# Optimization experiments

Hardware: AMD Instinct MI355X
Metric: run time of the kernel (lower is better)

## Reference

```python
import jax, jax.numpy as jnp
import numpy as np

N = 50000      # nodes
E = 800000     # edges (avg degree 16)
IN = 256       # in_feats
H = 128        # hidden_feats
C = 40         # out_feats == num classes (label dim)
LPA_ITERS = 10


def setup_inputs() -> dict:
    key = jax.random.key(0)
    ks = jax.random.split(key, 9)
    features = jax.random.normal(ks[0], (N, IN), dtype=jnp.float32)
    labels = jax.random.normal(ks[1], (N, C), dtype=jnp.float32)
    mask = jax.random.randint(ks[2], (N,), 0, 2) > 0          # bool [N]
    src = jax.random.randint(ks[3], (E,), 0, N, dtype=jnp.int32)
    dst = jax.random.randint(ks[4], (E,), 0, N, dtype=jnp.int32)
    W1 = jax.random.normal(ks[5], (IN, H), dtype=jnp.float32) * (1.0 / np.sqrt(IN))
    b1 = jnp.zeros((H,), dtype=jnp.float32)
    W2 = jax.random.normal(ks[6], (H, C), dtype=jnp.float32) * (1.0 / np.sqrt(H))
    b2 = jnp.zeros((C,), dtype=jnp.float32)
    return {"features": features, "labels": labels, "mask": mask,
            "src": src, "dst": dst, "W1": W1, "b1": b1, "W2": W2, "b2": b2}


def reference(features, labels, mask, src, dst, W1, b1, W2, b2):
    ones_e = jnp.ones((E,), dtype=jnp.float32)
    deg_out = jax.ops.segment_sum(ones_e, src, num_segments=N)  # out-degree
    deg_in = jax.ops.segment_sum(ones_e, dst, num_segments=N)   # in-degree
    norm_src = jnp.maximum(deg_out, 1.0) ** -0.5                 # DGL clamps deg>=1
    norm_dst = jnp.maximum(deg_in, 1.0) ** -0.5

    def gconv(x, W, b):
        # DGL GraphConv, norm='both': D_in^{-1/2} A^T D_out^{-1/2} (x W) + b
        h = (x @ W) * norm_src[:, None]                          # [N, d_out]
        agg = jax.ops.segment_sum(h[src], dst, num_segments=N)   # gather+scatter-add
        return agg * norm_dst[:, None] + b

    x = jax.nn.relu(gconv(features, W1, b1))
    # dropout identity in eval mode
    x = gconv(x, W2, b2)

    # Label propagation: adj[src,dst]=1 so (adj @ y)[i] = sum_{(i->j)} y[j]
    masked_labels = jnp.where(mask[:, None], labels, 0.0)

    def step(y, _):
        y = jax.ops.segment_sum(y[dst], src, num_segments=N)
        y = jnp.where(mask[:, None], labels, y)
        return y, None

    y, _ = jax.lax.scan(step, masked_labels, None, length=LPA_ITERS)
    return x, y
```

## Files before the change

### kernel.cpp

```cpp
#include <hip/hip_runtime.h>

#define Nn 50000
#define Ee 800000
#define INF_ 256
#define HID 128
#define NC 40
#define CAPD 48
#define CAPS 48
#define LPA_ITERS 10
#define NB 98
#define BSH 9
#define EPB 1024
#define NBLK ((Ee + EPB - 1) / EPB)
#define CAPB_D 10240
#define CAPB_S 6144

typedef __attribute__((ext_vector_type(8))) short bfrag;
typedef __attribute__((ext_vector_type(4))) float ffrag;

__device__ inline unsigned f2bf2(float a, float b) {
    unsigned ua = __float_as_uint(a); ua += 0x7FFFu + ((ua >> 16) & 1u);
    unsigned ub = __float_as_uint(b); ub += 0x7FFFu + ((ub >> 16) & 1u);
    return (ua >> 16) | (ub & 0xFFFF0000u);
}
__device__ inline unsigned short f2bf(float a) {
    unsigned ua = __float_as_uint(a); ua += 0x7FFFu + ((ua >> 16) & 1u);
    return (unsigned short)(ua >> 16);
}
__device__ inline float bf_lo(unsigned u) { return __uint_as_float(u << 16); }
__device__ inline float bf_hi(unsigned u) { return __uint_as_float(u & 0xFFFF0000u); }

__global__ void detect_fmt(const unsigned int* __restrict__ m, int* flag) {
    int i = blockIdx.x * blockDim.x + threadIdx.x;
    if (i < 12500) {
        if (m[i] > 1u) atomicOr(flag, 1);
    }
}

__device__ inline bool read_mask(const void* mask, int node, int fmt) {
    if (fmt) return ((const unsigned char*)mask)[node] != 0;
    return ((const int*)mask)[node] != 0;
}

__global__ __launch_bounds__(256) void bin_edges(
    const int* __restrict__ src, const int* __restrict__ dst,
    const void* __restrict__ mask, const int* __restrict__ flag,
    int* __restrict__ cnt_src,
    int* __restrict__ cur_d, int* __restrict__ cur_s,
    unsigned* __restrict__ bkt_d, unsigned* __restrict__ bkt_s) {
    __shared__ unsigned stage_d[EPB];
    __shared__ unsigned stage_s[EPB];
    __shared__ int hd[NB], od[NB + 1], cd[NB], gd_[NB];
    __shared__ int hs[NB], os_[NB + 1], cs_[NB], gs_[NB];
    __shared__ int sc[256];
    int tid = threadIdx.x;
    int e0 = blockIdx.x * EPB;
    int fmt = *flag;
    if (tid < NB) { hd[tid] = 0; hs[tid] = 0; }
    __syncthreads();

    int rs[EPB / 256], rd[EPB / 256];
    unsigned um = 0;
#pragma unroll
    for (int k = 0; k < EPB / 256; k++) {
        int e = e0 + tid + k * 256;
        rs[k] = -1; rd[k] = -1;
        if (e < Ee) {
            int s = src[e], d = dst[e];
            rs[k] = s; rd[k] = d;
            atomicAdd(&cnt_src[s], 1);
            atomicAdd(&hd[d >> BSH], 1);
            if (!read_mask(mask, s, fmt)) {
                um |= (1u << k);
                atomicAdd(&hs[s >> BSH], 1);
            }
        }
    }
    __syncthreads();
    {
        int seg = tid >> 7;
        int i = tid & 127;
        int v = 0;
        if (i < NB) v = seg ? hs[i] : hd[i];
        sc[tid] = v;
        __syncthreads();
#pragma unroll
        for (int offs = 1; offs < 128; offs <<= 1) {
            int add = (i >= offs) ? sc[tid - offs] : 0;
            __syncthreads();
            sc[tid] += add;
            __syncthreads();
        }
        if (i < NB) {
            int excl = i ? sc[tid - 1] : 0;
            if (seg == 0) od[i] = excl; else os_[i] = excl;
            if (i == NB - 1) {
                if (seg == 0) od[NB] = sc[tid]; else os_[NB] = sc[tid];
            }
        }
    }
    __syncthreads();
    if (tid < NB) {
        gd_[tid] = hd[tid] ? atomicAdd(&cur_d[tid], hd[tid]) : 0;
        gs_[tid] = hs[tid] ? atomicAdd(&cur_s[tid], hs[tid]) : 0;
        cd[tid] = od[tid];
        cs_[tid] = os_[tid];
    }
    __syncthreads();
#pragma unroll
    for (int k = 0; k < EPB / 256; k++) {
        if (rd[k] >= 0) {
            int p = atomicAdd(&cd[rd[k] >> BSH], 1);
            stage_d[p] = ((unsigned)rd[k] << 16) | (unsigned)rs[k];
            if (um & (1u << k)) {
                int q = atomicAdd(&cs_[rs[k] >> BSH], 1);
                stage_s[q] = ((unsigned)rs[k] << 16) | (unsigned)rd[k];
            }
        }
    }
    __syncthreads();
    int totd = od[NB];
    for (int i = tid; i < totd; i += 256) {
        int lo = 0, hi = NB;
        while (hi - lo > 1) {
            int mid = (lo + hi) >> 1;
            if (od[mid] <= i) lo = mid; else hi = mid;
        }
        int pos = gd_[lo] + (i - od[lo]);
        if (pos < CAPB_D) bkt_d[(size_t)lo * CAPB_D + pos] = stage_d[i];
    }
    int tots = os_[NB];
    for (int i = tid; i < tots; i += 256) {
        int lo = 0, hi = NB;
        while (hi - lo > 1) {
            int mid = (lo + hi) >> 1;
            if (os_[mid] <= i) lo = mid; else hi = mid;
        }
        int pos = gs_[lo] + (i - os_[lo]);
        if (pos < CAPB_S) bkt_s[(size_t)lo * CAPB_S + pos] = stage_s[i];
    }
}

__global__ __launch_bounds__(256) void build_csr_both(
    const unsigned* __restrict__ bkt_d, const int* __restrict__ cur_d,
    const unsigned* __restrict__ bkt_s, const int* __restrict__ cur_s,
    const void* __restrict__ mask, const int* __restrict__ flag,
    int* __restrict__ adj_dst, int* __restrict__ cnt_dst,
    int* __restrict__ adj_s, int* __restrict__ cnt_u, int* __restrict__ cnt_m) {
    __shared__ int lu[512], lm[512];
    int bb = blockIdx.x, tid = threadIdx.x;
    lu[tid] = 0; lu[tid + 256] = 0; lm[tid] = 0; lm[tid + 256] = 0;
    __syncthreads();
    if (bb < NB) {
        int b = bb;
        int n = cur_d[b]; if (n > CAPB_D) n = CAPB_D;
        int n0 = b << BSH;
        const unsigned* base = bkt_d + (size_t)b * CAPB_D;
        for (int i = tid; i < n; i += 256) {
            unsigned r = base[i];
            int d = r >> 16, s = r & 0xffff;
            int sl = atomicAdd(&lu[d - n0], 1);
            if (sl < CAPD) adj_dst[d * CAPD + sl] = s;
        }
        __syncthreads();
        int g0 = n0 + tid;
        if (g0 < Nn) cnt_dst[g0] = lu[tid];
        g0 += 256;
        if (g0 < Nn) cnt_dst[g0] = lu[tid + 256];
    } else {
        int b = bb - NB;
        int fmt = *flag;
        int n = cur_s[b]; if (n > CAPB_S) n = CAPB_S;
        int n0 = b << BSH;
        const unsigned* base = bkt_s + (size_t)b * CAPB_S;
        for (int i = tid; i < n; i += 256) {
            unsigned r = base[i];
            int s = r >> 16, d = r & 0xffff;
            if (read_mask(mask, d, fmt)) {
                int sl = atomicAdd(&lm[s - n0], 1);
                if (sl < CAPS) adj_s[s * CAPS + (CAPS - 1 - sl)] = d;
            } else {
                int sl = atomicAdd(&lu[s - n0], 1);
                if (sl < CAPS) adj_s[s * CAPS + sl] = d;
            }
        }
        __syncthreads();
        int g0 = n0 + tid;
        if (g0 < Nn) { cnt_u[g0] = lu[tid]; cnt_m[g0] = lm[tid]; }
        g0 += 256;
        if (g0 < Nn) { cnt_u[g0] = lu[tid + 256]; cnt_m[g0] = lm[tid + 256]; }
    }
}

__global__ void build_unmasked(const void* __restrict__ mask,
                               const int* __restrict__ flag,
                               int* n_un, int* __restrict__ ulist) {
    int i = blockIdx.x * blockDim.x + threadIdx.x;
    if (i < Nn) {
        if (!read_mask(mask, i, *flag)) {
            int p = atomicAdd(n_un, 1);
            ulist[p] = i;
        }
    }
}

__global__ void prep_w1t(const float* __restrict__ W1,
                         unsigned short* __restrict__ W1t) {
    int c = blockIdx.x;
    int k = threadIdx.x;
    W1t[c * INF_ + k] = f2bf(W1[(size_t)k * HID + c]);
}

#define G1_ROWS 64
__global__ __launch_bounds__(256) void gemm1(
    const float* __restrict__ feat, const unsigned short* __restrict__ W1t,
    const int* __restrict__ cnt_src, unsigned short* __restrict__ h1b) {
    __shared__ unsigned short lA[G1_ROWS * 32];
    __shared__ unsigned short lB[HID * 32];
    const int tid = threadIdx.x;
    const int row0 = blockIdx.x * G1_ROWS;
    const int w = tid >> 6;
    const int l = tid & 63;
    const int lane15 = l & 15;
    const int quad = l >> 4;
    const int rw0 = w * 16;

    ffrag acc[8];
#pragma unroll
    for (int t = 0; t < 8; t++) acc[t] = (ffrag){0.f, 0.f, 0.f, 0.f};

    for (int k0 = 0; k0 < INF_; k0 += 32) {
#pragma unroll
        for (int p = 0; p < 2; p++) {
            int idx = tid + p * 256;
            int r = idx >> 3, c4 = idx & 7;
            int grow = row0 + r;
            float4 v = make_float4(0.f, 0.f, 0.f, 0.f);
            if (grow < Nn)
                v = *(const float4*)(feat + (size_t)grow * INF_ + k0 + c4 * 4);
            uint2 pk;
            pk.x = f2bf2(v.x, v.y);
            pk.y = f2bf2(v.z, v.w);
            *(uint2*)((char*)lA + r * 64 + c4 * 8) = pk;
        }
#pragma unroll
        for (int p = 0; p < 2; p++) {
            int idx = tid + p * 256;
            int col = idx >> 2, q = idx & 3;
            uint4 v = *(const uint4*)((const char*)W1t + col * 512 + k0 * 2 + q * 16);
            *(uint4*)((char*)lB + col * 64 + q * 16) = v;
        }
        __syncthreads();
        int arow = rw0 + lane15;
        bfrag af = *(const bfrag*)((const char*)lA + arow * 64 + quad * 16);
#pragma unroll
        for (int t = 0; t < 8; t++) {
            int col = t * 16 + lane15;
            bfrag bf = *(const bfrag*)((const char*)lB + col * 64 + quad * 16);
            acc[t] = __builtin_amdgcn_mfma_f32_16x16x32_bf16(af, bf, acc[t], 0, 0, 0);
        }
        __syncthreads();
    }
    float nrm[4];
#pragma unroll
    for (int i = 0; i < 4; i++) {
        int grow = row0 + rw0 + quad * 4 + i;
        int dg = (grow < Nn) ? cnt_src[grow] : 1;
        nrm[i] = rsqrtf((float)(dg > 1 ? dg : 1));
    }
#pragma unroll
    for (int t = 0; t < 8; t++) {
#pragma unroll
        for (int i = 0; i < 4; i++) {
            int grow = row0 + rw0 + quad * 4 + i;
            if (grow < Nn)
                h1b[(size_t)grow * HID + t * 16 + lane15] = f2bf(acc[t][i] * nrm[i]);
        }
    }
}

__global__ __launch_bounds__(256) void agg_relu1(
    const uint4* __restrict__ h1b, const int* __restrict__ adj_dst,
    const int* __restrict__ cnt_dst, const float4* __restrict__ b1,
    float4* __restrict__ x1) {
    int node = blockIdx.x * 16 + (threadIdx.x >> 4);
    int l = threadIdx.x & 15;
    int dg = cnt_dst[node];
    int cnt = dg < CAPD ? dg : CAPD;
    const int* lst = adj_dst + (size_t)node * CAPD;
    float s0 = 0.f, s1 = 0.f, s2 = 0.f, s3 = 0.f;
    float s4 = 0.f, s5 = 0.f, s6 = 0.f, s7 = 0.f;
    int e = 0;
    for (; e + 8 <= cnt; e += 8) {
        uint4 u[8];
#pragma unroll
        for (int q = 0; q < 8; q++) u[q] = h1b[(size_t)lst[e + q] * 16 + l];
#pragma unroll
        for (int q = 0; q < 8; q++) {
            s0 += bf_lo(u[q].x); s1 += bf_hi(u[q].x);
            s2 += bf_lo(u[q].y); s3 += bf_hi(u[q].y);
            s4 += bf_lo(u[q].z); s5 += bf_hi(u[q].z);
            s6 += bf_lo(u[q].w); s7 += bf_hi(u[q].w);
        }
    }
    for (; e < cnt; e++) {
        uint4 u = h1b[(size_t)lst[e] * 16 + l];
        s0 += bf_lo(u.x); s1 += bf_hi(u.x);
        s2 += bf_lo(u.y); s3 += bf_hi(u.y);
        s4 += bf_lo(u.z); s5 += bf_hi(u.z);
        s6 += bf_lo(u.w); s7 += bf_hi(u.w);
    }
    float nrm = rsqrtf((float)(dg > 1 ? dg : 1));
    float4 bb0 = b1[l * 2], bb1 = b1[l * 2 + 1];
    float4 v0, v1;
    v0.x = fmaxf(s0 * nrm + bb0.x, 0.f);
    v0.y = fmaxf(s1 * nrm + bb0.y, 0.f);
    v0.z = fmaxf(s2 * nrm + bb0.z, 0.f);
    v0.w = fmaxf(s3 * nrm + bb0.w, 0.f);
    v1.x = fmaxf(s4 * nrm + bb1.x, 0.f);
    v1.y = fmaxf(s5 * nrm + bb1.y, 0.f);
    v1.z = fmaxf(s6 * nrm + bb1.z, 0.f);
    v1.w = fmaxf(s7 * nrm + bb1.w, 0.f);
    x1[(size_t)node * 32 + l * 2] = v0;
    x1[(size_t)node * 32 + l * 2 + 1] = v1;
}

__global__ __launch_bounds__(256) void gemm2(
    const float4* __restrict__ x1, const float4* __restrict__ W2,
    const int* __restrict__ cnt_src, unsigned* __restrict__ h2b) {
    __shared__ float lw[HID * NC];
    int tid = threadIdx.x;
    for (int i = tid; i < HID * NC / 4; i += 256)
        ((float4*)lw)[i] = W2[i];
    __syncthreads();
    int r = blockIdx.x * 256 + tid;
    if (r >= Nn) return;
    const float4* xr = x1 + (size_t)r * 32;
    float4 acc[10];
#pragma unroll
    for (int j = 0; j < 10; j++) acc[j] = make_float4(0.f, 0.f, 0.f, 0.f);
    for (int k4 = 0; k4 < 32; k4++) {
        float4 xv = xr[k4];
#pragma unroll
        for (int s = 0; s < 4; s++) {
            float x = s == 0 ? xv.x : (s == 1 ? xv.y : (s == 2 ? xv.z : xv.w));
            const float4* wrow = (const float4*)(lw + (k4 * 4 + s) * NC);
#pragma unroll
            for (int j = 0; j < 10; j++) {
                float4 w = wrow[j];
                acc[j].x += x * w.x; acc[j].y += x * w.y;
                acc[j].z += x * w.z; acc[j].w += x * w.w;
            }
        }
    }
    int dg = cnt_src[r];
    float nrm = rsqrtf((float)(dg > 1 ? dg : 1));
    uint2* out = (uint2*)(h2b + (size_t)r * 20);
#pragma unroll
    for (int j = 0; j < 10; j++) {
        uint2 pk;
        pk.x = f2bf2(acc[j].x * nrm, acc[j].y * nrm);
        pk.y = f2bf2(acc[j].z * nrm, acc[j].w * nrm);
        out[j] = pk;
    }
}

__global__ __launch_bounds__(320) void agg2(
    const uint2* __restrict__ h2b, const int* __restrict__ adj_dst,
    const int* __restrict__ cnt_dst, const float4* __restrict__ b2,
    float4* __restrict__ out_x) {
    int node = blockIdx.x * 32 + threadIdx.x / 10;
    int l = threadIdx.x % 10;
    if (node >= Nn) return;
    int dg = cnt_dst[node];
    int cnt = dg < CAPD ? dg : CAPD;
    const int* lst = adj_dst + (size_t)node * CAPD;
    float s0 = 0.f, s1 = 0.f, s2 = 0.f, s3 = 0.f;
    int e = 0;
    for (; e + 8 <= cnt; e += 8) {
        uint2 u[8];
#pragma unroll
        for (int q = 0; q < 8; q++) u[q] = h2b[(size_t)lst[e + q] * 10 + l];
#pragma unroll
        for (int q = 0; q < 8; q++) {
            s0 += bf_lo(u[q].x); s1 += bf_hi(u[q].x);
            s2 += bf_lo(u[q].y); s3 += bf_hi(u[q].y);
        }
    }
    for (; e + 4 <= cnt; e += 4) {
        uint2 u[4];
#pragma unroll
        for (int q = 0; q < 4; q++) u[q] = h2b[(size_t)lst[e + q] * 10 + l];
#pragma unroll
        for (int q = 0; q < 4; q++) {
            s0 += bf_lo(u[q].x); s1 += bf_hi(u[q].x);
            s2 += bf_lo(u[q].y); s3 += bf_hi(u[q].y);
        }
    }
    for (; e < cnt; e++) {
        uint2 u = h2b[(size_t)lst[e] * 10 + l];
        s0 += bf_lo(u.x); s1 += bf_hi(u.x);
        s2 += bf_lo(u.y); s3 += bf_hi(u.y);
    }
    float nrm = rsqrtf((float)(dg > 1 ? dg : 1));
    float4 bb = b2[l];
    float4 v;
    v.x = s0 * nrm + bb.x;
    v.y = s1 * nrm + bb.y;
    v.z = s2 * nrm + bb.z;
    v.w = s3 * nrm + bb.w;
    out_x[(size_t)node * 10 + l] = v;
}

__global__ void lpa_init(const float* __restrict__ labels, const void* mask,
                         const int* __restrict__ flag, float* __restrict__ out_y) {
    int g = blockIdx.x * blockDim.x + threadIdx.x;
    if (g >= Nn * NC) return;
    int node = g / NC;
    if (read_mask(mask, node, *flag)) out_y[g] = labels[g];
}

__global__ __launch_bounds__(320) void lpa_const(
    const float4* __restrict__ labels, const int* __restrict__ n_un,
    const int* __restrict__ ulist, const int* __restrict__ adj_s,
    const int* __restrict__ cnt_m, float4* __restrict__ sconst,
    uint2* __restrict__ y1b) {
    int g = blockIdx.x * 32 + threadIdx.x / 10;
    int l = threadIdx.x % 10;
    if (g >= *n_un) return;
    int u = ulist[g];
    int cm = cnt_m[u];
    int cnt = cm < CAPS ? cm : CAPS;
    const int* lst = adj_s + (size_t)u * CAPS + (CAPS - cnt);
    float4 s = make_float4(0.f, 0.f, 0.f, 0.f);
    int e = 0;
    for (; e + 8 <= cnt; e += 8) {
        float4 v[8];
#pragma unroll
        for (int q = 0; q < 8; q++) v[q] = labels[(size_t)lst[e + q] * 10 + l];
#pragma unroll
        for (int q = 0; q < 8; q++) {
            s.x += v[q].x; s.y += v[q].y; s.z += v[q].z; s.w += v[q].w;
        }
    }
    for (; e + 4 <= cnt; e += 4) {
        float4 v[4];
#pragma unroll
        for (int q = 0; q < 4; q++) v[q] = labels[(size_t)lst[e + q] * 10 + l];
#pragma unroll
        for (int q = 0; q < 4; q++) {
            s.x += v[q].x; s.y += v[q].y; s.z += v[q].z; s.w += v[q].w;
        }
    }
    for (; e < cnt; e++) {
        float4 a = labels[(size_t)lst[e] * 10 + l];
        s.x += a.x; s.y += a.y; s.z += a.z; s.w += a.w;
    }
    sconst[(size_t)u * 10 + l] = s;
    uint2 pk; pk.x = f2bf2(s.x, s.y); pk.y = f2bf2(s.z, s.w);
    y1b[(size_t)u * 10 + l] = pk;
}

__global__ __launch_bounds__(320) void lpa_mid(
    const uint2* __restrict__ ycur, const int* __restrict__ n_un,
    const int* __restrict__ ulist, const int* __restrict__ adj_s,
    const int* __restrict__ cnt_u, const float4* __restrict__ sconst,
    uint2* __restrict__ ynext) {
    int g = blockIdx.x * 32 + threadIdx.x / 10;
    int l = threadIdx.x % 10;
    if (g >= *n_un) return;
    int u = ulist[g];
    int cu = cnt_u[u];
    int cnt = cu < CAPS ? cu : CAPS;
    const int* lst = adj_s + (size_t)u * CAPS;
    float4 s = sconst[(size_t)u * 10 + l];
    int e = 0;
    for (; e + 8 <= cnt; e += 8) {
        uint2 v[8];
#pragma unroll
        for (int q = 0; q < 8; q++) v[q] = ycur[(size_t)lst[e + q] * 10 + l];
#pragma unroll
        for (int q = 0; q < 8; q++) {
            s.x += bf_lo(v[q].x); s.y += bf_hi(v[q].x);
            s.z += bf_lo(v[q].y); s.w += bf_hi(v[q].y);
        }
    }
    for (; e + 4 <= cnt; e += 4) {
        uint2 v[4];
#pragma unroll
        for (int q = 0; q < 4; q++) v[q] = ycur[(size_t)lst[e + q] * 10 + l];
#pragma unroll
        for (int q = 0; q < 4; q++) {
            s.x += bf_lo(v[q].x); s.y += bf_hi(v[q].x);
            s.z += bf_lo(v[q].y); s.w += bf_hi(v[q].y);
        }
    }
    for (; e < cnt; e++) {
        uint2 v = ycur[(size_t)lst[e] * 10 + l];
        s.x += bf_lo(v.x); s.y += bf_hi(v.x);
        s.z += bf_lo(v.y); s.w += bf_hi(v.y);
    }
    uint2 pk; pk.x = f2bf2(s.x, s.y); pk.y = f2bf2(s.z, s.w);
    ynext[(size_t)u * 10 + l] = pk;
}

__global__ __launch_bounds__(320) void lpa_last(
    const uint2* __restrict__ ycur, const int* __restrict__ n_un,
    const int* __restrict__ ulist, const int* __restrict__ adj_s,
    const int* __restrict__ cnt_u, const float4* __restrict__ sconst,
    float4* __restrict__ out_y) {
    int g = blockIdx.x * 32 + threadIdx.x / 10;
    int l = threadIdx.x % 10;
    if (g >= *n_un) return;
    int u = ulist[g];
    int cu = cnt_u[u];
    int cnt = cu < CAPS ? cu : CAPS;
    const int* lst = adj_s + (size_t)u * CAPS;
    float4 s = sconst[(size_t)u * 10 + l];
    int e = 0;
    for (; e + 8 <= cnt; e += 8) {
        uint2 v[8];
#pragma unroll
        for (int q = 0; q < 8; q++) v[q] = ycur[(size_t)lst[e + q] * 10 + l];
#pragma unroll
        for (int q = 0; q < 8; q++) {
            s.x += bf_lo(v[q].x); s.y += bf_hi(v[q].x);
            s.z += bf_lo(v[q].y); s.w += bf_hi(v[q].y);
        }
    }
    for (; e + 4 <= cnt; e += 4) {
        uint2 v[4];
#pragma unroll
        for (int q = 0; q < 4; q++) v[q] = ycur[(size_t)lst[e + q] * 10 + l];
#pragma unroll
        for (int q = 0; q < 4; q++) {
            s.x += bf_lo(v[q].x); s.y += bf_hi(v[q].x);
            s.z += bf_lo(v[q].y); s.w += bf_hi(v[q].y);
        }
    }
    for (; e < cnt; e++) {
        uint2 v = ycur[(size_t)lst[e] * 10 + l];
        s.x += bf_lo(v.x); s.y += bf_hi(v.x);
        s.z += bf_lo(v.y); s.w += bf_hi(v.y);
    }
    out_y[(size_t)u * 10 + l] = s;
}

extern "C" void kernel_launch(void* const* d_in, const int* in_sizes, int n_in,
                              void* d_out, int out_size, void* d_ws, size_t ws_size,
                              hipStream_t stream) {
    const float* feat   = (const float*)d_in[0];
    const float* labels = (const float*)d_in[1];
    const void*  mask   = d_in[2];
    const int*   src    = (const int*)d_in[3];
    const int*   dst    = (const int*)d_in[4];
    const float* W1     = (const float*)d_in[5];
    const float* b1     = (const float*)d_in[6];
    const float* W2     = (const float*)d_in[7];
    const float* b2     = (const float*)d_in[8];

    float* out_x = (float*)d_out;
    float* out_y = out_x + (size_t)Nn * NC;

    char* ws = (char*)d_ws;
    size_t off = 0;
    auto alloc = [&](size_t bytes) -> void* {
        void* p = ws + off;
        off += (bytes + 255) & ~(size_t)255;
        return p;
    };
    int* flag    = (int*)alloc(256);
    int* n_un    = flag + 1;
    int* cnt_src = (int*)alloc((size_t)Nn * 4);
    int* cur_d   = (int*)alloc(512);
    int* cur_s   = (int*)alloc(512);
    size_t zero_bytes = off;
    int* cnt_dst = (int*)alloc((size_t)Nn * 4);
    int* cnt_u   = (int*)alloc((size_t)Nn * 4);
    int* cnt_m   = (int*)alloc((size_t)Nn * 4);
    int* ulist   = (int*)alloc((size_t)Nn * 4);
    unsigned short* W1t = (unsigned short*)alloc((size_t)HID * INF_ * 2);
    char* uni = (char*)alloc((size_t)Nn * HID * 2);
    unsigned* bkt_d = (unsigned*)uni;
    unsigned* bkt_s = (unsigned*)(uni + (size_t)NB * CAPB_D * 4);
    unsigned short* h1b = (unsigned short*)uni;
    float* x1 = (float*)alloc((size_t)Nn * HID * 4);
    int* adj_s   = (int*)alloc((size_t)Nn * CAPS * 4);
    int* adj_dst = (int*)alloc((size_t)Nn * CAPD * 4);
    unsigned* h2b = (unsigned*)alloc((size_t)Nn * NC * 2);
    float* sconst = (float*)alloc((size_t)Nn * NC * 4);
    uint2* y1b = (uint2*)alloc((size_t)Nn * NC * 2);
    uint2* y2b = (uint2*)alloc((size_t)Nn * NC * 2);

    hipMemsetAsync(d_ws, 0, zero_bytes, stream);

    detect_fmt<<<49, 256, 0, stream>>>((const unsigned int*)mask, flag);
    prep_w1t<<<HID, INF_, 0, stream>>>(W1, W1t);
    bin_edges<<<NBLK, 256, 0, stream>>>(src, dst, mask, flag, cnt_src,
                                        cur_d, cur_s, bkt_d, bkt_s);
    build_csr_both<<<NB * 2, 256, 0, stream>>>(bkt_d, cur_d, bkt_s, cur_s,
                                               mask, flag, adj_dst, cnt_dst,
                                               adj_s, cnt_u, cnt_m);
    build_unmasked<<<196, 256, 0, stream>>>(mask, flag, n_un, ulist);

    gemm1<<<(Nn + G1_ROWS - 1) / G1_ROWS, 256, 0, stream>>>(feat, W1t, cnt_src, h1b);
    agg_relu1<<<Nn / 16, 256, 0, stream>>>((const uint4*)h1b, adj_dst, cnt_dst,
                                           (const float4*)b1, (float4*)x1);
    gemm2<<<196, 256, 0, stream>>>((const float4*)x1, (const float4*)W2,
                                   cnt_src, h2b);
    agg2<<<(Nn + 31) / 32, 320, 0, stream>>>((const uint2*)h2b, adj_dst, cnt_dst,
                                             (const float4*)b2, (float4*)out_x);

    lpa_init<<<(Nn * NC + 255) / 256, 256, 0, stream>>>(labels, mask, flag, out_y);
    lpa_const<<<(Nn + 31) / 32, 320, 0, stream>>>(
        (const float4*)labels, n_un, ulist, adj_s, cnt_m, (float4*)sconst, y1b);
    const uint2* cur = y1b;
    for (int i = 0; i < 8; i++) {
        uint2* nxt = (i & 1) ? y1b : y2b;
        lpa_mid<<<(Nn + 31) / 32, 320, 0, stream>>>(
            cur, n_un, ulist, adj_s, cnt_u, (const float4*)sconst, nxt);
        cur = nxt;
    }
    lpa_last<<<(Nn + 31) / 32, 320, 0, stream>>>(
        cur, n_un, ulist, adj_s, cnt_u, (const float4*)sconst, (float4*)out_y);
}
```

Before: 394.1 us.

## Replace two-pass bucketed CSR build with direct global-atomic edge scatter

Removes the bin_edges/build_csr_both bucketing pipeline and the separate build_unmasked kernel. A single kernel now reads edges as int4, uses global atomics on per-node counters to claim adjacency slots directly, and builds the unmasked-node list in the same launch. This saves two launches and the intermediate bucket round-trip, but replaces LDS atomics with many contended global atomics and scattered writes. The counter arrays are now zeroed by the memset instead of written by the build kernel.

Result: slower. 406.5 us (+3.1%).

```diff
diff --git a/kernel.cpp b/kernel.cpp
--- a/kernel.cpp
+++ b/kernel.cpp
@@ -8,12 +8,6 @@
 #define CAPD 48
 #define CAPS 48
 #define LPA_ITERS 10
-#define NB 98
-#define BSH 9
-#define EPB 1024
-#define NBLK ((Ee + EPB - 1) / EPB)
-#define CAPB_D 10240
-#define CAPB_S 6144
 
 typedef __attribute__((ext_vector_type(8))) short bfrag;
 typedef __attribute__((ext_vector_type(4))) float ffrag;
@@ -42,164 +36,39 @@
     return ((const int*)mask)[node] != 0;
 }
 
-__global__ __launch_bounds__(256) void bin_edges(
-    const int* __restrict__ src, const int* __restrict__ dst,
+__global__ __launch_bounds__(256) void scatter_edges(
+    const int4* __restrict__ src4, const int4* __restrict__ dst4,
     const void* __restrict__ mask, const int* __restrict__ flag,
-    int* __restrict__ cnt_src,
-    int* __restrict__ cur_d, int* __restrict__ cur_s,
-    unsigned* __restrict__ bkt_d, unsigned* __restrict__ bkt_s) {
-    __shared__ unsigned stage_d[EPB];
-    __shared__ unsigned stage_s[EPB];
-    __shared__ int hd[NB], od[NB + 1], cd[NB], gd_[NB];
-    __shared__ int hs[NB], os_[NB + 1], cs_[NB], gs_[NB];
-    __shared__ int sc[256];
-    int tid = threadIdx.x;
-    int e0 = blockIdx.x * EPB;
-    int fmt = *flag;
-    if (tid < NB) { hd[tid] = 0; hs[tid] = 0; }
-    __syncthreads();
-
-    int rs[EPB / 256], rd[EPB / 256];
-    unsigned um = 0;
-#pragma unroll
-    for (int k = 0; k < EPB / 256; k++) {
-        int e = e0 + tid + k * 256;
-        rs[k] = -1; rd[k] = -1;
-        if (e < Ee) {
-            int s = src[e], d = dst[e];
-            rs[k] = s; rd[k] = d;
-            atomicAdd(&cnt_src[s], 1);
-            atomicAdd(&hd[d >> BSH], 1);
-            if (!read_mask(mask, s, fmt)) {
-                um |= (1u << k);
-                atomicAdd(&hs[s >> BSH], 1);
-            }
-        }
-    }
-    __syncthreads();
-    {
-        int seg = tid >> 7;
-        int i = tid & 127;
-        int v = 0;
-        if (i < NB) v = seg ? hs[i] : hd[i];
-        sc[tid] = v;
-        __syncthreads();
-#pragma unroll
-        for (int offs = 1; offs < 128; offs <<= 1) {
-            int add = (i >= offs) ? sc[tid - offs] : 0;
-            __syncthreads();
-            sc[tid] += add;
-            __syncthreads();
-        }
-        if (i < NB) {
-            int excl = i ? sc[tid - 1] : 0;
-            if (seg == 0) od[i] = excl; else os_[i] = excl;
-            if (i == NB - 1) {
-                if (seg == 0) od[NB] = sc[tid]; else os_[NB] = sc[tid];
-            }
-        }
-    }
-    __syncthreads();
-    if (tid < NB) {
-        gd_[tid] = hd[tid] ? atomicAdd(&cur_d[tid], hd[tid]) : 0;
-        gs_[tid] = hs[tid] ? atomicAdd(&cur_s[tid], hs[tid]) : 0;
-        cd[tid] = od[tid];
-        cs_[tid] = os_[tid];
-    }
-    __syncthreads();
-#pragma unroll
-    for (int k = 0; k < EPB / 256; k++) {
-        if (rd[k] >= 0) {
-            int p = atomicAdd(&cd[rd[k] >> BSH], 1);
-            stage_d[p] = ((unsigned)rd[k] << 16) | (unsigned)rs[k];
-            if (um & (1u << k)) {
-                int q = atomicAdd(&cs_[rs[k] >> BSH], 1);
-                stage_s[q] = ((unsigned)rs[k] << 16) | (unsigned)rd[k];
-            }
-        }
-    }
-    __syncthreads();
-    int totd = od[NB];
-    for (int i = tid; i < totd; i += 256) {
-        int lo = 0, hi = NB;
-        while (hi - lo > 1) {
-            int mid = (lo + hi) >> 1;
-            if (od[mid] <= i) lo = mid; else hi = mid;
-        }
-        int pos = gd_[lo] + (i - od[lo]);
-        if (pos < CAPB_D) bkt_d[(size_t)lo * CAPB_D + pos] = stage_d[i];
-    }
-    int tots = os_[NB];
-    for (int i = tid; i < tots; i += 256) {
-        int lo = 0, hi = NB;
-        while (hi - lo > 1) {
-            int mid = (lo + hi) >> 1;
-            if (os_[mid] <= i) lo = mid; else hi = mid;
-        }
-        int pos = gs_[lo] + (i - os_[lo]);
-        if (pos < CAPB_S) bkt_s[(size_t)lo * CAPB_S + pos] = stage_s[i];
-    }
-}
-
-__global__ __launch_bounds__(256) void build_csr_both(
-    const unsigned* __restrict__ bkt_d, const int* __restrict__ cur_d,
-    const unsigned* __restrict__ bkt_s, const int* __restrict__ cur_s,
-    const void* __restrict__ mask, const int* __restrict__ flag,
+    int* __restrict__ cnt_src, int* __restrict__ n_un, int* __restrict__ ulist,
     int* __restrict__ adj_dst, int* __restrict__ cnt_dst,
     int* __restrict__ adj_s, int* __restrict__ cnt_u, int* __restrict__ cnt_m) {
-    __shared__ int lu[512], lm[512];
-    int bb = blockIdx.x, tid = threadIdx.x;
-    lu[tid] = 0; lu[tid + 256] = 0; lm[tid] = 0; lm[tid + 256] = 0;
-    __syncthreads();
-    if (bb < NB) {
-        int b = bb;
-        int n = cur_d[b]; if (n > CAPB_D) n = CAPB_D;
-        int n0 = b << BSH;
-        const unsigned* base = bkt_d + (size_t)b * CAPB_D;
-        for (int i = tid; i < n; i += 256) {
-            unsigned r = base[i];
-            int d = r >> 16, s = r & 0xffff;
-            int sl = atomicAdd(&lu[d - n0], 1);
-            if (sl < CAPD) adj_dst[d * CAPD + sl] = s;
-        }
-        __syncthreads();
-        int g0 = n0 + tid;
-        if (g0 < Nn) cnt_dst[g0] = lu[tid];
-        g0 += 256;
-        if (g0 < Nn) cnt_dst[g0] = lu[tid + 256];
-    } else {
-        int b = bb - NB;
-        int fmt = *flag;
-        int n = cur_s[b]; if (n > CAPB_S) n = CAPB_S;
-        int n0 = b << BSH;
-        const unsigned* base = bkt_s + (size_t)b * CAPB_S;
-        for (int i = tid; i < n; i += 256) {
-            unsigned r = base[i];
-            int s = r >> 16, d = r & 0xffff;
+    int t = blockIdx.x * 256 + threadIdx.x;
+    int fmt = *flag;
+    if (t < Nn) {
+        if (!read_mask(mask, t, fmt)) {
+            int p = atomicAdd(n_un, 1);
+            ulist[p] = t;
+        }
+    }
+    if (t * 4 >= Ee) return;
+    int4 sv = src4[t];
+    int4 dv = dst4[t];
+    int ss[4] = {sv.x, sv.y, sv.z, sv.w};
+    int dd[4] = {dv.x, dv.y, dv.z, dv.w};
+#pragma unroll
+    for (int k = 0; k < 4; k++) {
+        int s = ss[k], d = dd[k];
+        atomicAdd(&cnt_src[s], 1);
+        int p = atomicAdd(&cnt_dst[d], 1);
+        if (p < CAPD) adj_dst[d * CAPD + p] = s;
+        if (!read_mask(mask, s, fmt)) {
             if (read_mask(mask, d, fmt)) {
-                int sl = atomicAdd(&lm[s - n0], 1);
-                if (sl < CAPS) adj_s[s * CAPS + (CAPS - 1 - sl)] = d;
+                int q = atomicAdd(&cnt_m[s], 1);
+                if (q < CAPS) adj_s[s * CAPS + (CAPS - 1 - q)] = d;
             } else {
-                int sl = atomicAdd(&lu[s - n0], 1);
-                if (sl < CAPS) adj_s[s * CAPS + sl] = d;
+                int q = atomicAdd(&cnt_u[s], 1);
+                if (q < CAPS) adj_s[s * CAPS + q] = d;
             }
-        }
-        __syncthreads();
-        int g0 = n0 + tid;
-        if (g0 < Nn) { cnt_u[g0] = lu[tid]; cnt_m[g0] = lm[tid]; }
-        g0 += 256;
-        if (g0 < Nn) { cnt_u[g0] = lu[tid + 256]; cnt_m[g0] = lm[tid + 256]; }
-    }
-}
-
-__global__ void build_unmasked(const void* __restrict__ mask,
-                               const int* __restrict__ flag,
-                               int* n_un, int* __restrict__ ulist) {
-    int i = blockIdx.x * blockDim.x + threadIdx.x;
-    if (i < Nn) {
-        if (!read_mask(mask, i, *flag)) {
-            int p = atomicAdd(n_un, 1);
-            ulist[p] = i;
         }
     }
 }
@@ -572,18 +441,13 @@
     int* flag    = (int*)alloc(256);
     int* n_un    = flag + 1;
     int* cnt_src = (int*)alloc((size_t)Nn * 4);
-    int* cur_d   = (int*)alloc(512);
-    int* cur_s   = (int*)alloc(512);
-    size_t zero_bytes = off;
     int* cnt_dst = (int*)alloc((size_t)Nn * 4);
     int* cnt_u   = (int*)alloc((size_t)Nn * 4);
     int* cnt_m   = (int*)alloc((size_t)Nn * 4);
+    size_t zero_bytes = off;
     int* ulist   = (int*)alloc((size_t)Nn * 4);
     unsigned short* W1t = (unsigned short*)alloc((size_t)HID * INF_ * 2);
-    char* uni = (char*)alloc((size_t)Nn * HID * 2);
-    unsigned* bkt_d = (unsigned*)uni;
-    unsigned* bkt_s = (unsigned*)(uni + (size_t)NB * CAPB_D * 4);
-    unsigned short* h1b = (unsigned short*)uni;
+    unsigned short* h1b = (unsigned short*)alloc((size_t)Nn * HID * 2);
     float* x1 = (float*)alloc((size_t)Nn * HID * 4);
     int* adj_s   = (int*)alloc((size_t)Nn * CAPS * 4);
     int* adj_dst = (int*)alloc((size_t)Nn * CAPD * 4);
@@ -596,12 +460,9 @@
 
     detect_fmt<<<49, 256, 0, stream>>>((const unsigned int*)mask, flag);
     prep_w1t<<<HID, INF_, 0, stream>>>(W1, W1t);
-    bin_edges<<<NBLK, 256, 0, stream>>>(src, dst, mask, flag, cnt_src,
-                                        cur_d, cur_s, bkt_d, bkt_s);
-    build_csr_both<<<NB * 2, 256, 0, stream>>>(bkt_d, cur_d, bkt_s, cur_s,
-                                               mask, flag, adj_dst, cnt_dst,
-                                               adj_s, cnt_u, cnt_m);
-    build_unmasked<<<196, 256, 0, stream>>>(mask, flag, n_un, ulist);
+    scatter_edges<<<(Ee / 4 + 255) / 256, 256, 0, stream>>>(
+        (const int4*)src, (const int4*)dst, mask, flag,
+        cnt_src, n_un, ulist, adj_dst, cnt_dst, adj_s, cnt_u, cnt_m);
 
     gemm1<<<(Nn + G1_ROWS - 1) / G1_ROWS, 256, 0, stream>>>(feat, W1t, cnt_src, h1b);
     agg_relu1<<<Nn / 16, 256, 0, stream>>>((const uint4*)h1b, adj_dst, cnt_dst,
```
